# Kernel tuning notes

Hardware: AMD Instinct MI355X
Metric: run time of the kernel (lower is better)

## Reference

```python
import jax, jax.numpy as jnp
import numpy as np

B, S, D = 4, 2048, 1024


def setup_inputs() -> dict:
    key = jax.random.key(0)
    ks = jax.random.split(key, 9)
    scale = 1.0 / np.sqrt(D)
    q = jax.random.normal(ks[0], (B, S, D), dtype=jnp.float32)
    k = jax.random.normal(ks[1], (B, S, D), dtype=jnp.float32)
    v = jax.random.normal(ks[2], (B, S, D), dtype=jnp.float32)
    w_q = jax.random.uniform(ks[3], (D, D), jnp.float32, -scale, scale)
    b_q = jax.random.uniform(ks[4], (D,), jnp.float32, -scale, scale)
    w_k = jax.random.uniform(ks[5], (D, D), jnp.float32, -scale, scale)
    b_k = jax.random.uniform(ks[6], (D,), jnp.float32, -scale, scale)
    w_v = jax.random.uniform(ks[7], (D, D), jnp.float32, -scale, scale)
    b_v = jax.random.uniform(ks[8], (D,), jnp.float32, -scale, scale)
    # additive causal mask: 0 on/below diagonal, -1e9 above
    causal = jnp.where(jnp.tril(jnp.ones((S, S), dtype=bool)), 0.0, -1e9)
    mask = causal[None, :, :].astype(jnp.float32)  # [1, S, S]
    return {"q": q, "k": k, "v": v, "mask": mask,
            "w_q": w_q, "b_q": b_q, "w_k": w_k, "b_k": b_k,
            "w_v": w_v, "b_v": b_v}


def reference(q, k, v, mask, w_q, b_q, w_k, b_k, w_v, b_v):
    # nn.Linear: x @ W^T + b
    query = jnp.einsum('bsd,ed->bse', q, w_q) + b_q  # [B,S,D]
    key_ = jnp.einsum('bsd,ed->bse', k, w_k) + b_k
    value = jnp.einsum('bsd,ed->bse', v, w_v) + b_v
    inv_sqrt_dk = 1.0 / jnp.sqrt(jnp.asarray(D, dtype=query.dtype))
    att = jnp.einsum('bqd,bkd->bqk', query, key_) * inv_sqrt_dk  # [B,S,S]
    att = att + mask
    score = jax.nn.softmax(att, axis=-1)
    return jnp.einsum('bqk,bkd->bqd', score, value)  # [B,S,D]
```

## Files before the change

kernel.cpp:

```cpp
#include <hip/hip_runtime.h>
#include <hip/hip_bf16.h>

#define SS 2048
#define DD 1024
#define NB 4

typedef __attribute__((ext_vector_type(8))) short  bf8;
typedef __attribute__((ext_vector_type(4))) float  f32x4;

static __device__ __forceinline__ unsigned short f2bf(float f) {
    unsigned u = __float_as_uint(f);
    u += 0x7fffu + ((u >> 16) & 1u);
    return (unsigned short)(u >> 16);
}

static __device__ __forceinline__ void gload_lds16(const void* g, void* lds) {
    __builtin_amdgcn_global_load_lds((__attribute__((address_space(1))) void*)g,
                                     (__attribute__((address_space(3))) void*)lds,
                                     16, 0, 0);
}

__global__ __launch_bounds__(256)
void cvt3(const float* __restrict__ a, const float* __restrict__ b, const float* __restrict__ c,
          unsigned short* __restrict__ oa, unsigned short* __restrict__ ob,
          unsigned short* __restrict__ oc, int n4) {
    int i = blockIdx.x * 256 + threadIdx.x;
    if (i >= n4) return;
    const float* in = blockIdx.y == 0 ? a : blockIdx.y == 1 ? b : c;
    unsigned short* out = blockIdx.y == 0 ? oa : blockIdx.y == 1 ? ob : oc;
    float4 v = ((const float4*)in)[i];
    ushort4 o;
    o.x = f2bf(v.x); o.y = f2bf(v.y); o.z = f2bf(v.z); o.w = f2bf(v.w);
    ((ushort4*)out)[i] = o;
}

#define BM 128
#define BN 128
#define BK 32

template<int MODE>
__global__ __launch_bounds__(256, 2)
void gemm_bt(const unsigned short* __restrict__ A0p, const unsigned short* __restrict__ B0p,
             const float* __restrict__ bias0,
             const unsigned short* __restrict__ A1p, const unsigned short* __restrict__ B1p,
             const float* __restrict__ bias1,
             const unsigned short* __restrict__ A2p, const unsigned short* __restrict__ B2p,
             const float* __restrict__ bias2,
             void* __restrict__ Cout)
{
    constexpr int LDA = (MODE == 3) ? 2048 : 1024;
    constexpr int LDB = (MODE == 3) ? 2048 : 1024;
    constexpr int GX  = (MODE == 2) ? 16 : 8;
    constexpr int NWG = (MODE == 0) ? 512 : (MODE == 2) ? 256 : 192;
    constexpr int CPX = NWG >> 3;

    int bx, by;
    {
        int f  = (int)blockIdx.y * GX + (int)blockIdx.x;
        int f2 = (f & 7) * CPX + (f >> 3);
        bx = f2 % GX; by = f2 / GX;
    }
    const int bz = blockIdx.z;
    if (MODE == 2 && bx > by) return;

    const unsigned short* A;
    const unsigned short* Bm;
    const float* bias = nullptr;
    int len, qt = 0, nsp = 1;
    if (MODE == 0) {
        A    = (bz == 0 ? A0p : bz == 1 ? A1p : A2p) + (size_t)by * BM * LDA;
        Bm   = (bz == 0 ? B0p : bz == 1 ? B1p : B2p) + (size_t)bx * BN * LDB;
        bias = bz == 0 ? bias0 : bz == 1 ? bias1 : bias2;
        len  = 1024;
    } else if (MODE == 2) {
        A   = A0p + (size_t)bz * SS * DD + (size_t)by * BM * LDA;
        Bm  = B0p + (size_t)bz * SS * DD + (size_t)bx * BN * LDB;
        len = 1024;
    } else {
        int seg = 0;
        if (by < 8) { qt = by; nsp = 1; }
        else        { qt = 8 + ((by - 8) >> 1); seg = (by - 8) & 1; nsp = 2; }
        int ktot = (qt + 1) * 128, hk = ktot >> 1;
        int kst  = (nsp == 2 && seg) ? hk : 0;
        len = (nsp == 1) ? ktot : hk;
        A  = A0p + (size_t)bz * SS * SS + (size_t)qt * BM * LDA + kst;
        Bm = B0p + (size_t)bz * DD * SS + (size_t)bx * BN * LDB + kst;
    }

    __shared__ __align__(16) unsigned short As[BM * BK];
    __shared__ __align__(16) unsigned short Bs[BN * BK];

    const int t = threadIdx.x;
    const int l = t & 63;
    const int w = t >> 6;
    const int wr = w >> 1, wc = w & 1;

    const int c0 = t, c1 = t + 256;
    const int r0 = c0 >> 2, k0 = (c0 & 3) * 8;
    const int r1 = c1 >> 2, k1 = (c1 & 3) * 8;

    f32x4 zero = {0.f, 0.f, 0.f, 0.f};
    f32x4 acc[4][4];
    #pragma unroll
    for (int i = 0; i < 4; i++)
        #pragma unroll
        for (int j = 0; j < 4; j++) acc[i][j] = zero;

    const int ar = wr * 64 + (l & 15);
    const int br = wc * 64 + (l & 15);
    const int kc = (l >> 4) * 8;

    for (int kk = 0; kk < len; kk += BK) {
        gload_lds16(A + (size_t)r0 * LDA + kk + k0, &As[c0 * 8]);
        gload_lds16(A + (size_t)r1 * LDA + kk + k1, &As[c1 * 8]);
        gload_lds16(Bm + (size_t)r0 * LDB + kk + k0, &Bs[c0 * 8]);
        gload_lds16(Bm + (size_t)r1 * LDB + kk + k1, &Bs[c1 * 8]);
        __syncthreads();
        bf8 af[4], bfr[4];
        #pragma unroll
        for (int i = 0; i < 4; i++) af[i]  = *(const bf8*)&As[(ar + i * 16) * BK + kc];
        #pragma unroll
        for (int j = 0; j < 4; j++) bfr[j] = *(const bf8*)&Bs[(br + j * 16) * BK + kc];
        #pragma unroll
        for (int i = 0; i < 4; i++)
            #pragma unroll
            for (int j = 0; j < 4; j++)
                acc[i][j] = __builtin_amdgcn_mfma_f32_16x16x32_bf16(af[i], bfr[j], acc[i][j], 0, 0, 0);
        __syncthreads();
    }

    const int mb = ((MODE == 3) ? qt : by) * BM + wr * 64;
    const int nb = bx * BN + wc * 64;

    if (MODE == 0) {
        float bv[4];
        #pragma unroll
        for (int j = 0; j < 4; j++) bv[j] = bias[nb + j * 16 + (l & 15)];
        if (bz < 2) {
            unsigned short* C = (unsigned short*)Cout + (size_t)bz * NB * SS * DD;
            #pragma unroll
            for (int i = 0; i < 4; i++) {
                int m0 = mb + i * 16 + ((l >> 4) << 2);
                #pragma unroll
                for (int j = 0; j < 4; j++) {
                    int n = nb + j * 16 + (l & 15);
                    #pragma unroll
                    for (int r = 0; r < 4; r++)
                        C[(size_t)(m0 + r) * DD + n] = f2bf(acc[i][j][r] + bv[j]);
                }
            }
        } else {
            unsigned short* C = (unsigned short*)Cout + (size_t)2 * NB * SS * DD;
            int batch = (by * BM) >> 11;
            #pragma unroll
            for (int i = 0; i < 4; i++) {
                int s = (mb - batch * SS) + i * 16 + ((l >> 4) << 2);
                #pragma unroll
                for (int j = 0; j < 4; j++) {
                    int n = nb + j * 16 + (l & 15);
                    ushort4 pk;
                    pk.x = f2bf(acc[i][j][0] + bv[j]);
                    pk.y = f2bf(acc[i][j][1] + bv[j]);
                    pk.z = f2bf(acc[i][j][2] + bv[j]);
                    pk.w = f2bf(acc[i][j][3] + bv[j]);
                    *(ushort4*)&C[(size_t)batch * DD * SS + (size_t)n * SS + s] = pk;
                }
            }
        }
    } else if (MODE == 2) {
        float* C = (float*)Cout + (size_t)bz * SS * SS;
        #pragma unroll
        for (int i = 0; i < 4; i++) {
            int m0 = mb + i * 16 + ((l >> 4) << 2);
            #pragma unroll
            for (int j = 0; j < 4; j++) {
                int n = nb + j * 16 + (l & 15);
                #pragma unroll
                for (int r = 0; r < 4; r++)
                    C[(size_t)(m0 + r) * SS + n] = acc[i][j][r] * 0.03125f;
            }
        }
    } else {
        float* C = (float*)Cout + (size_t)bz * SS * DD;
        #pragma unroll
        for (int i = 0; i < 4; i++) {
            int m0 = mb + i * 16 + ((l >> 4) << 2);
            #pragma unroll
            for (int j = 0; j < 4; j++) {
                int n = nb + j * 16 + (l & 15);
                if (nsp == 1) {
                    #pragma unroll
                    for (int r = 0; r < 4; r++)
                        C[(size_t)(m0 + r) * DD + n] = acc[i][j][r];
                } else {
                    #pragma unroll
                    for (int r = 0; r < 4; r++)
                        atomicAdd(&C[(size_t)(m0 + r) * DD + n], acc[i][j][r]);
                }
            }
        }
    }
}

__global__ __launch_bounds__(256)
void softmax_causal(const float* __restrict__ Sb, unsigned short* __restrict__ P) {
    __shared__ float tmp[8];
    int row = blockIdx.x;
    int b = row >> 11, q = row & 2047;
    const float* s = Sb + ((size_t)b * SS + q) * SS;
    unsigned short* p = P + ((size_t)b * SS + q) * SS;
    int len  = q + 1;
    int len4 = len >> 2;
    int wlen = ((q >> 7) + 1) << 7;

    float mx = -3e38f;
    for (int i = threadIdx.x; i < len4; i += 256) {
        float4 v = ((const float4*)s)[i];
        mx = fmaxf(fmaxf(fmaxf(mx, v.x), v.y), fmaxf(v.z, v.w));
    }
    for (int i = (len4 << 2) + threadIdx.x; i < len; i += 256) mx = fmaxf(mx, s[i]);
    #pragma unroll
    for (int o = 32; o; o >>= 1) mx = fmaxf(mx, __shfl_xor(mx, o));
    if ((threadIdx.x & 63) == 0) tmp[threadIdx.x >> 6] = mx;
    __syncthreads();
    mx = fmaxf(fmaxf(tmp[0], tmp[1]), fmaxf(tmp[2], tmp[3]));

    float sum = 0.f;
    for (int i = threadIdx.x; i < len4; i += 256) {
        float4 v = ((const float4*)s)[i];
        sum += __expf(v.x - mx) + __expf(v.y - mx) + __expf(v.z - mx) + __expf(v.w - mx);
    }
    for (int i = (len4 << 2) + threadIdx.x; i < len; i += 256) sum += __expf(s[i] - mx);
    #pragma unroll
    for (int o = 32; o; o >>= 1) sum += __shfl_xor(sum, o);
    if ((threadIdx.x & 63) == 0) tmp[4 + (threadIdx.x >> 6)] = sum;
    __syncthreads();
    sum = tmp[4] + tmp[5] + tmp[6] + tmp[7];
    float inv = 1.f / sum;

    for (int i4 = threadIdx.x; i4 < (wlen >> 2); i4 += 256) {
        int i = i4 << 2;
        float4 v = ((const float4*)s)[i4];
        ushort4 o;
        o.x = (i     < len) ? f2bf(__expf(v.x - mx) * inv) : (unsigned short)0;
        o.y = (i + 1 < len) ? f2bf(__expf(v.y - mx) * inv) : (unsigned short)0;
        o.z = (i + 2 < len) ? f2bf(__expf(v.z - mx) * inv) : (unsigned short)0;
        o.w = (i + 3 < len) ? f2bf(__expf(v.w - mx) * inv) : (unsigned short)0;
        *(ushort4*)&p[i] = o;
    }
}

extern "C" void kernel_launch(void* const* d_in, const int* in_sizes, int n_in,
                              void* d_out, int out_size, void* d_ws, size_t ws_size,
                              hipStream_t stream) {
    constexpr size_t NX = (size_t)NB * SS * DD;
    constexpr size_t NW = (size_t)DD * DD;

    const float* q   = (const float*)d_in[0];
    const float* k   = (const float*)d_in[1];
    const float* v   = (const float*)d_in[2];
    const float* w_q = (const float*)d_in[4];
    const float* b_q = (const float*)d_in[5];
    const float* w_k = (const float*)d_in[6];
    const float* b_k = (const float*)d_in[7];
    const float* w_v = (const float*)d_in[8];
    const float* b_v = (const float*)d_in[9];
    float* out = (float*)d_out;

    char* ws = (char*)d_ws;
    size_t off = 0;
    auto take = [&](size_t bytes) { char* p = ws + off; off += (bytes + 255) & ~(size_t)255; return p; };
    unsigned short* qb  = (unsigned short*)take(NX * 2);
    unsigned short* kb  = (unsigned short*)take(NX * 2);
    unsigned short* vb  = (unsigned short*)take(NX * 2);
    unsigned short* wqb = (unsigned short*)take(NW * 2);
    unsigned short* wkb = (unsigned short*)take(NW * 2);
    unsigned short* wvb = (unsigned short*)take(NW * 2);
    unsigned short* QKV = (unsigned short*)take(NX * 2 * 3);
    float*          Sb  = (float*)take((size_t)NB * SS * SS * 4);
    unsigned short* Qp  = QKV;
    unsigned short* Kp  = QKV + NX;
    unsigned short* VpT = QKV + 2 * NX;
    unsigned short* P   = qb;

    dim3 blk(256);
    hipMemsetAsync(d_out, 0, NB * (size_t)SS * DD * 4, stream);
    cvt3<<<dim3(NX / 4 / 256, 3), blk, 0, stream>>>(q, k, v, qb, kb, vb, (int)(NX / 4));
    cvt3<<<dim3(NW / 4 / 256, 3), blk, 0, stream>>>(w_q, w_k, w_v, wqb, wkb, wvb, (int)(NW / 4));

    gemm_bt<0><<<dim3(8, 64, 3), blk, 0, stream>>>(
        qb, wqb, b_q, kb, wkb, b_k, vb, wvb, b_v, QKV);

    gemm_bt<2><<<dim3(16, 16, 4), blk, 0, stream>>>(
        Qp, Kp, nullptr, nullptr, nullptr, nullptr, nullptr, nullptr, nullptr, Sb);

    softmax_causal<<<dim3(NB * SS), blk, 0, stream>>>(Sb, P);

    gemm_bt<3><<<dim3(8, 24, 4), blk, 0, stream>>>(
        P, VpT, nullptr, nullptr, nullptr, nullptr, nullptr, nullptr, nullptr, out);
}
```

Before: 219.4 us.

## Use BK=64 swizzled LDS tiles, bf16 score matrix, online softmax, partial memset

Doubles the GEMM K-tile to 64 and adds an XOR swizzle to the LDS layout, so there are half as many barriers per K and fewer bank conflicts. The QK^T score buffer is stored as bf16 instead of fp32, halving its write and read traffic. The softmax becomes a single-pass online max/sum followed by the normalisation pass, which drops one full read of each row. The output memset is narrowed to the rows that use atomic accumulation. Storing scores in bf16 lowers precision before the softmax.

```diff
diff --git a/kernel.cpp b/kernel.cpp
--- a/kernel.cpp
+++ b/kernel.cpp
@@ -12,6 +12,9 @@
     unsigned u = __float_as_uint(f);
     u += 0x7fffu + ((u >> 16) & 1u);
     return (unsigned short)(u >> 16);
+}
+static __device__ __forceinline__ float bf2f(unsigned short u) {
+    return __uint_as_float((unsigned)u << 16);
 }
 
 static __device__ __forceinline__ void gload_lds16(const void* g, void* lds) {
@@ -36,7 +39,7 @@
 
 #define BM 128
 #define BN 128
-#define BK 32
+#define BK 64
 
 template<int MODE>
 __global__ __launch_bounds__(256, 2)
@@ -95,9 +98,8 @@
     const int w = t >> 6;
     const int wr = w >> 1, wc = w & 1;
 
-    const int c0 = t, c1 = t + 256;
-    const int r0 = c0 >> 2, k0 = (c0 & 3) * 8;
-    const int r1 = c1 >> 2, k1 = (c1 & 3) * 8;
+    const int srow0 = t >> 3;
+    const int sswz  = (t & 7) ^ ((t >> 3) & 7);
 
     f32x4 zero = {0.f, 0.f, 0.f, 0.f};
     f32x4 acc[4][4];
@@ -108,24 +110,37 @@
 
     const int ar = wr * 64 + (l & 15);
     const int br = wc * 64 + (l & 15);
-    const int kc = (l >> 4) * 8;
+    const int j0 = l >> 4;
 
     for (int kk = 0; kk < len; kk += BK) {
-        gload_lds16(A + (size_t)r0 * LDA + kk + k0, &As[c0 * 8]);
-        gload_lds16(A + (size_t)r1 * LDA + kk + k1, &As[c1 * 8]);
-        gload_lds16(Bm + (size_t)r0 * LDB + kk + k0, &Bs[c0 * 8]);
-        gload_lds16(Bm + (size_t)r1 * LDB + kk + k1, &Bs[c1 * 8]);
+        #pragma unroll
+        for (int j = 0; j < 4; ++j) {
+            int r = srow0 + 32 * j;
+            gload_lds16(A + (size_t)r * LDA + kk + sswz * 8,
+                        (char*)As + (t + 256 * j) * 16);
+            gload_lds16(Bm + (size_t)r * LDB + kk + sswz * 8,
+                        (char*)Bs + (t + 256 * j) * 16);
+        }
         __syncthreads();
-        bf8 af[4], bfr[4];
-        #pragma unroll
-        for (int i = 0; i < 4; i++) af[i]  = *(const bf8*)&As[(ar + i * 16) * BK + kc];
-        #pragma unroll
-        for (int j = 0; j < 4; j++) bfr[j] = *(const bf8*)&Bs[(br + j * 16) * BK + kc];
-        #pragma unroll
-        for (int i = 0; i < 4; i++)
-            #pragma unroll
-            for (int j = 0; j < 4; j++)
-                acc[i][j] = __builtin_amdgcn_mfma_f32_16x16x32_bf16(af[i], bfr[j], acc[i][j], 0, 0, 0);
+        #pragma unroll
+        for (int ks = 0; ks < 2; ++ks) {
+            bf8 af[4], bfr[4];
+            #pragma unroll
+            for (int i = 0; i < 4; i++) {
+                int r = ar + i * 16;
+                af[i] = *(const bf8*)((char*)As + r * 128 + (((j0 + ks * 4) ^ (r & 7)) << 4));
+            }
+            #pragma unroll
+            for (int j = 0; j < 4; j++) {
+                int r = br + j * 16;
+                bfr[j] = *(const bf8*)((char*)Bs + r * 128 + (((j0 + ks * 4) ^ (r & 7)) << 4));
+            }
+            #pragma unroll
+            for (int i = 0; i < 4; i++)
+                #pragma unroll
+                for (int j = 0; j < 4; j++)
+                    acc[i][j] = __builtin_amdgcn_mfma_f32_16x16x32_bf16(af[i], bfr[j], acc[i][j], 0, 0, 0);
+        }
         __syncthreads();
     }
 
@@ -168,7 +183,7 @@
             }
         }
     } else if (MODE == 2) {
-        float* C = (float*)Cout + (size_t)bz * SS * SS;
+        unsigned short* C = (unsigned short*)Cout + (size_t)bz * SS * SS;
         #pragma unroll
         for (int i = 0; i < 4; i++) {
             int m0 = mb + i * 16 + ((l >> 4) << 2);
@@ -177,7 +192,7 @@
                 int n = nb + j * 16 + (l & 15);
                 #pragma unroll
                 for (int r = 0; r < 4; r++)
-                    C[(size_t)(m0 + r) * SS + n] = acc[i][j][r] * 0.03125f;
+                    C[(size_t)(m0 + r) * SS + n] = f2bf(acc[i][j][r] * 0.03125f);
             }
         }
     } else {
@@ -203,50 +218,71 @@
 }
 
 __global__ __launch_bounds__(256)
-void softmax_causal(const float* __restrict__ Sb, unsigned short* __restrict__ P) {
-    __shared__ float tmp[8];
+void softmax_causal(const unsigned short* __restrict__ Sb, unsigned short* __restrict__ P) {
+    __shared__ float tm[4], tl[4];
     int row = blockIdx.x;
     int b = row >> 11, q = row & 2047;
-    const float* s = Sb + ((size_t)b * SS + q) * SS;
+    const unsigned short* s = Sb + ((size_t)b * SS + q) * SS;
     unsigned short* p = P + ((size_t)b * SS + q) * SS;
     int len  = q + 1;
-    int len4 = len >> 2;
+    int len8 = len >> 3;
     int wlen = ((q >> 7) + 1) << 7;
 
-    float mx = -3e38f;
-    for (int i = threadIdx.x; i < len4; i += 256) {
-        float4 v = ((const float4*)s)[i];
-        mx = fmaxf(fmaxf(fmaxf(mx, v.x), v.y), fmaxf(v.z, v.w));
-    }
-    for (int i = (len4 << 2) + threadIdx.x; i < len; i += 256) mx = fmaxf(mx, s[i]);
+    float m = -3e38f, lsum = 0.f;
+    for (int i8 = threadIdx.x; i8 < len8; i8 += 256) {
+        ushort4 u0 = ((const ushort4*)s)[i8 * 2];
+        ushort4 u1 = ((const ushort4*)s)[i8 * 2 + 1];
+        float v[8] = {bf2f(u0.x), bf2f(u0.y), bf2f(u0.z), bf2f(u0.w),
+                      bf2f(u1.x), bf2f(u1.y), bf2f(u1.z), bf2f(u1.w)};
+        float cm = v[0];
+        #pragma unroll
+        for (int e = 1; e < 8; ++e) cm = fmaxf(cm, v[e]);
+        float cs = 0.f;
+        #pragma unroll
+        for (int e = 0; e < 8; ++e) cs += __expf(v[e] - cm);
+        float nm = fmaxf(m, cm);
+        lsum = lsum * __expf(m - nm) + cs * __expf(cm - nm);
+        m = nm;
+    }
+    for (int i = (len8 << 3) + threadIdx.x; i < len; i += 256) {
+        float v = bf2f(s[i]);
+        float nm = fmaxf(m, v);
+        lsum = lsum * __expf(m - nm) + __expf(v - nm);
+        m = nm;
+    }
     #pragma unroll
-    for (int o = 32; o; o >>= 1) mx = fmaxf(mx, __shfl_xor(mx, o));
-    if ((threadIdx.x & 63) == 0) tmp[threadIdx.x >> 6] = mx;
+    for (int o = 32; o; o >>= 1) {
+        float om = __shfl_xor(m, o);
+        float ol = __shfl_xor(lsum, o);
+        float nm = fmaxf(m, om);
+        lsum = lsum * __expf(m - nm) + ol * __expf(om - nm);
+        m = nm;
+    }
+    if ((threadIdx.x & 63) == 0) { tm[threadIdx.x >> 6] = m; tl[threadIdx.x >> 6] = lsum; }
     __syncthreads();
-    mx = fmaxf(fmaxf(tmp[0], tmp[1]), fmaxf(tmp[2], tmp[3]));
-
-    float sum = 0.f;
-    for (int i = threadIdx.x; i < len4; i += 256) {
-        float4 v = ((const float4*)s)[i];
-        sum += __expf(v.x - mx) + __expf(v.y - mx) + __expf(v.z - mx) + __expf(v.w - mx);
-    }
-    for (int i = (len4 << 2) + threadIdx.x; i < len; i += 256) sum += __expf(s[i] - mx);
-    #pragma unroll
-    for (int o = 32; o; o >>= 1) sum += __shfl_xor(sum, o);
-    if ((threadIdx.x & 63) == 0) tmp[4 + (threadIdx.x >> 6)] = sum;
-    __syncthreads();
-    sum = tmp[4] + tmp[5] + tmp[6] + tmp[7];
-    float inv = 1.f / sum;
-
-    for (int i4 = threadIdx.x; i4 < (wlen >> 2); i4 += 256) {
-        int i = i4 << 2;
-        float4 v = ((const float4*)s)[i4];
-        ushort4 o;
-        o.x = (i     < len) ? f2bf(__expf(v.x - mx) * inv) : (unsigned short)0;
-        o.y = (i + 1 < len) ? f2bf(__expf(v.y - mx) * inv) : (unsigned short)0;
-        o.z = (i + 2 < len) ? f2bf(__expf(v.z - mx) * inv) : (unsigned short)0;
-        o.w = (i + 3 < len) ? f2bf(__expf(v.w - mx) * inv) : (unsigned short)0;
-        *(ushort4*)&p[i] = o;
+    {
+        float gm = fmaxf(fmaxf(tm[0], tm[1]), fmaxf(tm[2], tm[3]));
+        float gl = tl[0] * __expf(tm[0] - gm) + tl[1] * __expf(tm[1] - gm)
+                 + tl[2] * __expf(tm[2] - gm) + tl[3] * __expf(tm[3] - gm);
+        m = gm; lsum = gl;
+    }
+    float inv = 1.f / lsum;
+
+    for (int i8 = threadIdx.x; i8 < (wlen >> 3); i8 += 256) {
+        int i = i8 << 3;
+        ushort4 u0 = ((const ushort4*)s)[i8 * 2];
+        ushort4 u1 = ((const ushort4*)s)[i8 * 2 + 1];
+        ushort4 o0, o1;
+        o0.x = (i     < len) ? f2bf(__expf(bf2f(u0.x) - m) * inv) : (unsigned short)0;
+        o0.y = (i + 1 < len) ? f2bf(__expf(bf2f(u0.y) - m) * inv) : (unsigned short)0;
+        o0.z = (i + 2 < len) ? f2bf(__expf(bf2f(u0.z) - m) * inv) : (unsigned short)0;
+        o0.w = (i + 3 < len) ? f2bf(__expf(bf2f(u0.w) - m) * inv) : (unsigned short)0;
+        o1.x = (i + 4 < len) ? f2bf(__expf(bf2f(u1.x) - m) * inv) : (unsigned short)0;
+        o1.y = (i + 5 < len) ? f2bf(__expf(bf2f(u1.y) - m) * inv) : (unsigned short)0;
+        o1.z = (i + 6 < len) ? f2bf(__expf(bf2f(u1.z) - m) * inv) : (unsigned short)0;
+        o1.w = (i + 7 < len) ? f2bf(__expf(bf2f(u1.w) - m) * inv) : (unsigned short)0;
+        ((ushort4*)p)[i8 * 2]     = o0;
+        ((ushort4*)p)[i8 * 2 + 1] = o1;
     }
 }
 
@@ -277,14 +313,14 @@
     unsigned short* wkb = (unsigned short*)take(NW * 2);
     unsigned short* wvb = (unsigned short*)take(NW * 2);
     unsigned short* QKV = (unsigned short*)take(NX * 2 * 3);
-    float*          Sb  = (float*)take((size_t)NB * SS * SS * 4);
+    unsigned short* Sb  = (unsigned short*)take((size_t)NB * SS * SS * 2);
     unsigned short* Qp  = QKV;
-    unsigned short* Kp  = QKV + NX;
     unsigned short* VpT = QKV + 2 * NX;
     unsigned short* P   = qb;
 
     dim3 blk(256);
-    hipMemsetAsync(d_out, 0, NB * (size_t)SS * DD * 4, stream);
+    for (int b = 0; b < NB; ++b)
+        hipMemsetAsync(out + ((size_t)b * SS + 1024) * DD, 0, (size_t)1024 * DD * 4, stream);
     cvt3<<<dim3(NX / 4 / 256, 3), blk, 0, stream>>>(q, k, v, qb, kb, vb, (int)(NX / 4));
     cvt3<<<dim3(NW / 4 / 256, 3), blk, 0, stream>>>(w_q, w_k, w_v, wqb, wkb, wvb, (int)(NW / 4));
 
@@ -292,7 +328,7 @@
         qb, wqb, b_q, kb, wkb, b_k, vb, wvb, b_v, QKV);
 
     gemm_bt<2><<<dim3(16, 16, 4), blk, 0, stream>>>(
-        Qp, Kp, nullptr, nullptr, nullptr, nullptr, nullptr, nullptr, nullptr, Sb);
+        Qp, Qp + NX, nullptr, nullptr, nullptr, nullptr, nullptr, nullptr, nullptr, Sb);
 
     softmax_causal<<<dim3(NB * SS), blk, 0, stream>>>(Sb, P);
 
```

New measurement: 190.5 us. 1.15x faster.
